# Kernel optimization log

Hardware: AMD Instinct MI355X
Metric: run time of the kernel (lower is better)

## Reference

```python
import jax, jax.numpy as jnp
import numpy as np

D_K = 128


def setup_inputs() -> dict:
    key = jax.random.key(0)
    kq, kk, kv = jax.random.split(key, 3)
    S = 8192
    Query = jax.random.normal(kq, (S, D_K), dtype=jnp.float32)
    Key = jax.random.normal(kk, (S, D_K), dtype=jnp.float32)
    Value = jax.random.normal(kv, (S, D_K), dtype=jnp.float32)
    return {"Query": Query, "Key": Key, "Value": Value}


def reference(Query, Key, Value):
    # scaled dot-product attention, unmasked (masked=False default)
    scale = 1.0 / jnp.sqrt(jnp.asarray(D_K, dtype=jnp.float32))
    scores = jnp.matmul(Query, Key.T) * scale          # [S, S]
    attn = jax.nn.softmax(scores, axis=1)              # softmax over keys (dim=1 on 2-D)
    delta_E = jnp.matmul(attn, Value)                  # [S, d_k]
    return delta_E
```

## Files before the change

### kernel.cpp

```cpp
#include <hip/hip_runtime.h>

#define S_LEN 8192
#define D_KK  128
#define SCALE 0.08838834764831845f

typedef __bf16 bf16x2 __attribute__((ext_vector_type(2)));
typedef __bf16 bf16x4 __attribute__((ext_vector_type(4)));
typedef __bf16 bf16x8 __attribute__((ext_vector_type(8)));
typedef float  f32x16 __attribute__((ext_vector_type(16)));
typedef _Float16 half_t;

__global__ __launch_bounds__(256) void prep_kv_23450521436217(
    const float* __restrict__ K,
    const float* __restrict__ V,
    __bf16* __restrict__ Kf,
    __bf16* __restrict__ Vf)
{
    const int tid = threadIdx.x;
    const int t   = blockIdx.x;
    __shared__ __bf16 T[32][140];

    const float* ktile = K + (size_t)t * 32 * D_KK;
    const float* vtile = V + (size_t)t * 32 * D_KK;

    const int row = tid & 31;
    const int cp  = tid >> 5;
    #pragma unroll
    for (int i = 0; i < 2; ++i) {
        int c = cp * 2 + i;
        int s = c >> 1, hi = c & 1;
        const float* src = ktile + row * D_KK + c * 8;
        float4 a = *(const float4*)(src);
        float4 b = *(const float4*)(src + 4);
        bf16x8 o;
        o[0]=(__bf16)a.x; o[1]=(__bf16)a.y; o[2]=(__bf16)a.z; o[3]=(__bf16)a.w;
        o[4]=(__bf16)b.x; o[5]=(__bf16)b.y; o[6]=(__bf16)b.z; o[7]=(__bf16)b.w;
        *(bf16x8*)(Kf + (size_t)(t * 8 + s) * 512 + hi * 256 + row * 8) = o;
    }

    #pragma unroll
    for (int i = 0; i < 4; ++i) {
        int f4 = tid + i * 256;
        float4 v = ((const float4*)vtile)[f4];
        int r = f4 >> 5, cc = (f4 & 31) << 2;
        bf16x4 b;
        b[0]=(__bf16)v.x; b[1]=(__bf16)v.y; b[2]=(__bf16)v.z; b[3]=(__bf16)v.w;
        *(bf16x4*)(&T[r][cc]) = b;
    }
    __syncthreads();

    #pragma unroll
    for (int i = 0; i < 2; ++i) {
        int idx  = tid + i * 256;
        int frag = idx >> 6, lane = idx & 63;
        int hi = lane >> 5, l5 = lane & 31;
        int d = frag >> 1, h = frag & 1;
        bf16x8 o;
        #pragma unroll
        for (int j = 0; j < 8; ++j) o[j] = T[16 * h + 8 * hi + j][32 * d + l5];
        *(bf16x8*)(Vf + (size_t)(t * 8 + frag) * 512 + lane * 8) = o;
    }
}

__global__ __launch_bounds__(512, 2) void attn_part_23450521436217(
    const float*  __restrict__ Q,
    const __bf16* __restrict__ Kf,
    const __bf16* __restrict__ Vf,
    half_t* __restrict__ P16,
    float*  __restrict__ Mp,
    float*  __restrict__ Lp)
{
    const int tid  = threadIdx.x;
    const int wave = tid >> 6;
    const int lane = tid & 63;
    const int l5   = lane & 31;
    const int hi   = lane >> 5;

    const int ks   = blockIdx.x & 7;
    const int qt   = blockIdx.x >> 3;
    const int qsub = qt * 8 + wave;
    const int qrow = qsub * 32 + l5;

    __shared__ __align__(16) __bf16 Klds[2][4096];

    bf16x8 qf[8];
    #pragma unroll
    for (int s = 0; s < 8; ++s) {
        const float* qp = Q + (size_t)qrow * D_KK + s * 16 + hi * 8;
        float4 a = *(const float4*)(qp);
        float4 b = *(const float4*)(qp + 4);
        bf16x8 f;
        f[0]=(__bf16)(a.x*SCALE); f[1]=(__bf16)(a.y*SCALE);
        f[2]=(__bf16)(a.z*SCALE); f[3]=(__bf16)(a.w*SCALE);
        f[4]=(__bf16)(b.x*SCALE); f[5]=(__bf16)(b.y*SCALE);
        f[6]=(__bf16)(b.z*SCALE); f[7]=(__bf16)(b.w*SCALE);
        qf[s] = f;
    }

    f32x16 oacc[4];
    #pragma unroll
    for (int d = 0; d < 4; ++d) oacc[d] = f32x16{};
    float m_run = -1e30f, l_run = 0.0f;

    const __bf16* kbase = Kf + (size_t)(ks * 32) * 4096;
    const __bf16* vfp   = Vf + (size_t)(ks * 32) * 4096 + lane * 8;

    {
        const __bf16* src = kbase + wave * 512 + lane * 8;
        __builtin_amdgcn_global_load_lds(
            (const __attribute__((address_space(1))) void*)src,
            (__attribute__((address_space(3))) void*)&Klds[0][wave * 512],
            16, 0, 0);
    }
    __syncthreads();

    for (int it = 0; it < 32; ++it) {
        const int cur = it & 1;

        if (it < 31) {
            const __bf16* src = kbase + (size_t)(it + 1) * 4096 + wave * 512 + lane * 8;
            __builtin_amdgcn_global_load_lds(
                (const __attribute__((address_space(1))) void*)src,
                (__attribute__((address_space(3))) void*)&Klds[cur ^ 1][wave * 512],
                16, 0, 0);
        }

        const __bf16* vt = vfp + (size_t)it * 4096;
        bf16x8 vb[8];
        #pragma unroll
        for (int f = 0; f < 8; ++f) vb[f] = *(const bf16x8*)(vt + f * 512);

        f32x16 c = f32x16{};
        __builtin_amdgcn_s_setprio(1);
        #pragma unroll
        for (int s = 0; s < 8; ++s) {
            bf16x8 kf = *(const bf16x8*)(&Klds[cur][s * 512 + lane * 8]);
            c = __builtin_amdgcn_mfma_f32_32x32x16_bf16(kf, qf[s], c, 0, 0, 0);
        }
        __builtin_amdgcn_s_setprio(0);

        float x0 = fmaxf(c[0], c[8]),  x1 = fmaxf(c[1], c[9]);
        float x2 = fmaxf(c[2], c[10]), x3 = fmaxf(c[3], c[11]);
        float x4 = fmaxf(c[4], c[12]), x5 = fmaxf(c[5], c[13]);
        float x6 = fmaxf(c[6], c[14]), x7 = fmaxf(c[7], c[15]);
        float y0 = fmaxf(fmaxf(x0, x4), fmaxf(x1, x5));
        float y1 = fmaxf(fmaxf(x2, x6), fmaxf(x3, x7));
        float tmax = fmaxf(y0, y1);
        tmax = fmaxf(tmax, __shfl_xor(tmax, 32));
        if (__any(tmax > m_run + 8.0f)) {
            float mnew  = fmaxf(m_run, tmax);
            float alpha = __expf(m_run - mnew);
            #pragma unroll
            for (int d = 0; d < 4; ++d) oacc[d] *= alpha;
            l_run *= alpha;
            m_run  = mnew;
        }
        float p[16];
        #pragma unroll
        for (int r = 0; r < 16; ++r) p[r] = __expf(c[r] - m_run);
        float s0a = (p[0]+p[1]) + (p[2]+p[3]),   s1a = (p[4]+p[5]) + (p[6]+p[7]);
        float s2a = (p[8]+p[9]) + (p[10]+p[11]), s3a = (p[12]+p[13]) + (p[14]+p[15]);
        float ps = (s0a + s1a) + (s2a + s3a);
        ps += __shfl_xor(ps, 32);
        l_run += ps;

        unsigned pk[8];
        #pragma unroll
        for (int tq = 0; tq < 8; ++tq) {
            bf16x2 w; w[0] = (__bf16)p[2*tq]; w[1] = (__bf16)p[2*tq+1];
            pk[tq] = __builtin_bit_cast(unsigned, w);
        }
        asm volatile("v_permlane32_swap_b32 %0, %1" : "+v"(pk[0]), "+v"(pk[2]));
        asm volatile("v_permlane32_swap_b32 %0, %1" : "+v"(pk[1]), "+v"(pk[3]));
        asm volatile("v_permlane32_swap_b32 %0, %1" : "+v"(pk[4]), "+v"(pk[6]));
        asm volatile("v_permlane32_swap_b32 %0, %1" : "+v"(pk[5]), "+v"(pk[7]));
        union { unsigned u[4]; bf16x8 f; } b0, b1;
        b0.u[0]=pk[0]; b0.u[1]=pk[1]; b0.u[2]=pk[2]; b0.u[3]=pk[3];
        b1.u[0]=pk[4]; b1.u[1]=pk[5]; b1.u[2]=pk[6]; b1.u[3]=pk[7];

        __builtin_amdgcn_s_setprio(1);
        #pragma unroll
        for (int d = 0; d < 4; ++d) {
            oacc[d] = __builtin_amdgcn_mfma_f32_32x32x16_bf16(vb[2*d+0], b0.f,
                                                              oacc[d], 0,0,0);
            oacc[d] = __builtin_amdgcn_mfma_f32_32x32x16_bf16(vb[2*d+1], b1.f,
                                                              oacc[d], 0,0,0);
        }
        __builtin_amdgcn_s_setprio(0);

        __syncthreads();
    }

    if (lane < 32) {
        Mp[ks * S_LEN + qrow] = m_run;
        Lp[ks * S_LEN + qrow] = l_run;
    }
    half_t* pb = P16 + (size_t)(ks * 256 + qsub) * (128 * 32);
    #pragma unroll
    for (int d = 0; d < 4; ++d)
        #pragma unroll
        for (int reg = 0; reg < 16; ++reg) {
            int drow = d * 32 + (reg & 3) + 8 * (reg >> 2) + 4 * hi;
            pb[drow * 32 + l5] = (half_t)oacc[d][reg];
        }
}

__global__ __launch_bounds__(256) void attn_merge_23450521436217(
    const half_t* __restrict__ P16,
    const float*  __restrict__ Mp,
    const float*  __restrict__ Lp,
    float* __restrict__ O)
{
    const int tid  = threadIdx.x;
    const int qsub = blockIdx.x;

    __shared__ float W[8][32];
    __shared__ float Li[32];
    __shared__ float Ot[128][33];

    if (tid < 32) {
        const int qrow = qsub * 32 + tid;
        float m[8], l[8];
        #pragma unroll
        for (int ks = 0; ks < 8; ++ks) {
            m[ks] = Mp[ks * S_LEN + qrow];
            l[ks] = Lp[ks * S_LEN + qrow];
        }
        float M = m[0];
        #pragma unroll
        for (int ks = 1; ks < 8; ++ks) M = fmaxf(M, m[ks]);
        float L = 0.0f;
        #pragma unroll
        for (int ks = 0; ks < 8; ++ks) {
            float w = __expf(m[ks] - M);
            W[ks][tid] = w;
            L += l[ks] * w;
        }
        Li[tid] = 1.0f / L;
    }
    __syncthreads();

    const int q  = tid & 31;
    const int dg = tid >> 5;
    #pragma unroll
    for (int j = 0; j < 16; ++j) {
        const int d = dg * 16 + j;
        float acc = 0.0f;
        #pragma unroll
        for (int ks = 0; ks < 8; ++ks)
            acc += W[ks][q] *
                   (float)P16[(size_t)(ks * 256 + qsub) * (128 * 32) + d * 32 + q];
        Ot[d][q] = acc;
    }
    __syncthreads();

    const int qq = tid >> 3;
    const int dv = (tid & 7) * 16;
    const float il = Li[qq];
    float* op = O + (size_t)(qsub * 32 + qq) * D_KK + dv;
    #pragma unroll
    for (int i = 0; i < 4; ++i) {
        float4 o;
        o.x = Ot[dv + i*4 + 0][qq] * il;
        o.y = Ot[dv + i*4 + 1][qq] * il;
        o.z = Ot[dv + i*4 + 2][qq] * il;
        o.w = Ot[dv + i*4 + 3][qq] * il;
        ((float4*)op)[i] = o;
    }
}

extern "C" void kernel_launch(void* const* d_in, const int* in_sizes, int n_in,
                              void* d_out, int out_size, void* d_ws, size_t ws_size,
                              hipStream_t stream) {
    const float* Q = (const float*)d_in[0];
    const float* K = (const float*)d_in[1];
    const float* V = (const float*)d_in[2];
    float* O = (float*)d_out;

    char* ws = (char*)d_ws;
    const size_t kf_b = (size_t)S_LEN * D_KK * 2;
    __bf16* Kf = (__bf16*)(ws);
    __bf16* Vf = (__bf16*)(ws + kf_b);
    float*  Mp = (float*) (ws + 2 * kf_b);
    float*  Lp = (float*) (ws + 2 * kf_b + 8 * S_LEN * 4);
    half_t* P16= (half_t*)(ws + 2 * kf_b + 16 * S_LEN * 4);

    hipLaunchKernelGGL(prep_kv_23450521436217, dim3(S_LEN/32), dim3(256), 0, stream,
                       K, V, Kf, Vf);
    hipLaunchKernelGGL(attn_part_23450521436217, dim3(256), dim3(512), 0, stream,
                       Q, Kf, Vf, P16, Mp, Lp);
    hipLaunchKernelGGL(attn_merge_23450521436217, dim3(S_LEN/32), dim3(256), 0, stream,
                       P16, Mp, Lp, O);
}
```

Baseline: 63.83 us.

## Stage V tiles through double-buffered LDS and switch softmax to exp2 domain

V tiles are now streamed into a second double-buffered LDS array with async global-to-LDS loads, alongside K. Previously every wave fetched its own V fragments from global memory straight into registers, so the same data was loaded eight times per block. Separately, log2(e) is folded into the Q scale so the softmax can use exp2f instead of __expf, and the rescale threshold becomes 11.5, which is 8 in natural-log units. The change doubles LDS use per block, which may lower occupancy, and adds LDS reads in the PV stage.

```diff
diff --git a/kernel.cpp b/kernel.cpp
--- a/kernel.cpp
+++ b/kernel.cpp
@@ -2,7 +2,7 @@
 
 #define S_LEN 8192
 #define D_KK  128
-#define SCALE 0.08838834764831845f
+#define SCALE2 (0.08838834764831845f * 1.44269504088896340f)
 
 typedef __bf16 bf16x2 __attribute__((ext_vector_type(2)));
 typedef __bf16 bf16x4 __attribute__((ext_vector_type(4)));
@@ -82,6 +82,7 @@
     const int qrow = qsub * 32 + l5;
 
     __shared__ __align__(16) __bf16 Klds[2][4096];
+    __shared__ __align__(16) __bf16 Vlds[2][4096];
 
     bf16x8 qf[8];
     #pragma unroll
@@ -90,10 +91,10 @@
         float4 a = *(const float4*)(qp);
         float4 b = *(const float4*)(qp + 4);
         bf16x8 f;
-        f[0]=(__bf16)(a.x*SCALE); f[1]=(__bf16)(a.y*SCALE);
-        f[2]=(__bf16)(a.z*SCALE); f[3]=(__bf16)(a.w*SCALE);
-        f[4]=(__bf16)(b.x*SCALE); f[5]=(__bf16)(b.y*SCALE);
-        f[6]=(__bf16)(b.z*SCALE); f[7]=(__bf16)(b.w*SCALE);
+        f[0]=(__bf16)(a.x*SCALE2); f[1]=(__bf16)(a.y*SCALE2);
+        f[2]=(__bf16)(a.z*SCALE2); f[3]=(__bf16)(a.w*SCALE2);
+        f[4]=(__bf16)(b.x*SCALE2); f[5]=(__bf16)(b.y*SCALE2);
+        f[6]=(__bf16)(b.z*SCALE2); f[7]=(__bf16)(b.w*SCALE2);
         qf[s] = f;
     }
 
@@ -103,14 +104,19 @@
     float m_run = -1e30f, l_run = 0.0f;
 
     const __bf16* kbase = Kf + (size_t)(ks * 32) * 4096;
-    const __bf16* vfp   = Vf + (size_t)(ks * 32) * 4096 + lane * 8;
+    const __bf16* vbase = Vf + (size_t)(ks * 32) * 4096;
 
     {
-        const __bf16* src = kbase + wave * 512 + lane * 8;
+        const __bf16* ksrc = kbase + wave * 512 + lane * 8;
         __builtin_amdgcn_global_load_lds(
-            (const __attribute__((address_space(1))) void*)src,
+            (const __attribute__((address_space(1))) void*)ksrc,
             (__attribute__((address_space(3))) void*)&Klds[0][wave * 512],
             16, 0, 0);
+        const __bf16* vsrc = vbase + wave * 512 + lane * 8;
+        __builtin_amdgcn_global_load_lds(
+            (const __attribute__((address_space(1))) void*)vsrc,
+            (__attribute__((address_space(3))) void*)&Vlds[0][wave * 512],
+            16, 0, 0);
     }
     __syncthreads();
 
@@ -118,17 +124,17 @@
         const int cur = it & 1;
 
         if (it < 31) {
-            const __bf16* src = kbase + (size_t)(it + 1) * 4096 + wave * 512 + lane * 8;
+            const __bf16* ksrc = kbase + (size_t)(it + 1) * 4096 + wave * 512 + lane * 8;
             __builtin_amdgcn_global_load_lds(
-                (const __attribute__((address_space(1))) void*)src,
+                (const __attribute__((address_space(1))) void*)ksrc,
                 (__attribute__((address_space(3))) void*)&Klds[cur ^ 1][wave * 512],
                 16, 0, 0);
-        }
-
-        const __bf16* vt = vfp + (size_t)it * 4096;
-        bf16x8 vb[8];
-        #pragma unroll
-        for (int f = 0; f < 8; ++f) vb[f] = *(const bf16x8*)(vt + f * 512);
+            const __bf16* vsrc = vbase + (size_t)(it + 1) * 4096 + wave * 512 + lane * 8;
+            __builtin_amdgcn_global_load_lds(
+                (const __attribute__((address_space(1))) void*)vsrc,
+                (__attribute__((address_space(3))) void*)&Vlds[cur ^ 1][wave * 512],
+                16, 0, 0);
+        }
 
         f32x16 c = f32x16{};
         __builtin_amdgcn_s_setprio(1);
@@ -147,9 +153,9 @@
         float y1 = fmaxf(fmaxf(x2, x6), fmaxf(x3, x7));
         float tmax = fmaxf(y0, y1);
         tmax = fmaxf(tmax, __shfl_xor(tmax, 32));
-        if (__any(tmax > m_run + 8.0f)) {
+        if (__any(tmax > m_run + 11.5f)) {
             float mnew  = fmaxf(m_run, tmax);
-            float alpha = __expf(m_run - mnew);
+            float alpha = exp2f(m_run - mnew);
             #pragma unroll
             for (int d = 0; d < 4; ++d) oacc[d] *= alpha;
             l_run *= alpha;
@@ -157,7 +163,7 @@
         }
         float p[16];
         #pragma unroll
-        for (int r = 0; r < 16; ++r) p[r] = __expf(c[r] - m_run);
+        for (int r = 0; r < 16; ++r) p[r] = exp2f(c[r] - m_run);
         float s0a = (p[0]+p[1]) + (p[2]+p[3]),   s1a = (p[4]+p[5]) + (p[6]+p[7]);
         float s2a = (p[8]+p[9]) + (p[10]+p[11]), s3a = (p[12]+p[13]) + (p[14]+p[15]);
         float ps = (s0a + s1a) + (s2a + s3a);
@@ -181,9 +187,11 @@
         __builtin_amdgcn_s_setprio(1);
         #pragma unroll
         for (int d = 0; d < 4; ++d) {
-            oacc[d] = __builtin_amdgcn_mfma_f32_32x32x16_bf16(vb[2*d+0], b0.f,
+            bf16x8 v0 = *(const bf16x8*)(&Vlds[cur][(2*d)     * 512 + lane * 8]);
+            bf16x8 v1 = *(const bf16x8*)(&Vlds[cur][(2*d + 1) * 512 + lane * 8]);
+            oacc[d] = __builtin_amdgcn_mfma_f32_32x32x16_bf16(v0, b0.f,
                                                               oacc[d], 0,0,0);
-            oacc[d] = __builtin_amdgcn_mfma_f32_32x32x16_bf16(vb[2*d+1], b1.f,
+            oacc[d] = __builtin_amdgcn_mfma_f32_32x32x16_bf16(v1, b1.f,
                                                               oacc[d], 0,0,0);
         }
         __builtin_amdgcn_s_setprio(0);
@@ -232,7 +240,7 @@
         float L = 0.0f;
         #pragma unroll
         for (int ks = 0; ks < 8; ++ks) {
-            float w = __expf(m[ks] - M);
+            float w = exp2f(m[ks] - M);
             W[ks][tid] = w;
             L += l[ks] * w;
         }
```

New measurement: 73.03 us. 1.14x slower.

## Process two K/V subtiles per barrier and switch softmax to exp2 domain

Applied to the files above, without the earlier changes.

The main loop now stages two 32-key K subtiles per LDS buffer and runs 16 iterations instead of 32. This halves the number of __syncthreads barriers and prefetches twice as much K data per step. Q is pre-scaled by log2(e) so the softmax and the merge weights can use exp2f instead of __expf, and the rescale threshold is raised to 11.5 to match the base-2 domain. LDS use doubles and register pressure rises because two sets of V fragments are held per iteration, which may lower occupancy.

```diff
diff --git a/kernel.cpp b/kernel.cpp
--- a/kernel.cpp
+++ b/kernel.cpp
@@ -2,7 +2,7 @@
 
 #define S_LEN 8192
 #define D_KK  128
-#define SCALE 0.08838834764831845f
+#define SCALE2 (0.08838834764831845f * 1.44269504088896340f)
 
 typedef __bf16 bf16x2 __attribute__((ext_vector_type(2)));
 typedef __bf16 bf16x4 __attribute__((ext_vector_type(4)));
@@ -81,7 +81,7 @@
     const int qsub = qt * 8 + wave;
     const int qrow = qsub * 32 + l5;
 
-    __shared__ __align__(16) __bf16 Klds[2][4096];
+    __shared__ __align__(16) __bf16 Klds[2][2][4096];
 
     bf16x8 qf[8];
     #pragma unroll
@@ -90,10 +90,10 @@
         float4 a = *(const float4*)(qp);
         float4 b = *(const float4*)(qp + 4);
         bf16x8 f;
-        f[0]=(__bf16)(a.x*SCALE); f[1]=(__bf16)(a.y*SCALE);
-        f[2]=(__bf16)(a.z*SCALE); f[3]=(__bf16)(a.w*SCALE);
-        f[4]=(__bf16)(b.x*SCALE); f[5]=(__bf16)(b.y*SCALE);
-        f[6]=(__bf16)(b.z*SCALE); f[7]=(__bf16)(b.w*SCALE);
+        f[0]=(__bf16)(a.x*SCALE2); f[1]=(__bf16)(a.y*SCALE2);
+        f[2]=(__bf16)(a.z*SCALE2); f[3]=(__bf16)(a.w*SCALE2);
+        f[4]=(__bf16)(b.x*SCALE2); f[5]=(__bf16)(b.y*SCALE2);
+        f[6]=(__bf16)(b.z*SCALE2); f[7]=(__bf16)(b.w*SCALE2);
         qf[s] = f;
     }
 
@@ -105,91 +105,110 @@
     const __bf16* kbase = Kf + (size_t)(ks * 32) * 4096;
     const __bf16* vfp   = Vf + (size_t)(ks * 32) * 4096 + lane * 8;
 
-    {
-        const __bf16* src = kbase + wave * 512 + lane * 8;
+    #pragma unroll
+    for (int st = 0; st < 2; ++st) {
+        const __bf16* src = kbase + (size_t)st * 4096 + wave * 512 + lane * 8;
         __builtin_amdgcn_global_load_lds(
             (const __attribute__((address_space(1))) void*)src,
-            (__attribute__((address_space(3))) void*)&Klds[0][wave * 512],
+            (__attribute__((address_space(3))) void*)&Klds[0][st][wave * 512],
             16, 0, 0);
     }
     __syncthreads();
 
-    for (int it = 0; it < 32; ++it) {
+#define SUBTILE(CUR, ST, IT, VB)                                               \
+    {                                                                          \
+        f32x16 c = f32x16{};                                                   \
+        __builtin_amdgcn_s_setprio(1);                                         \
+        _Pragma("unroll")                                                      \
+        for (int s = 0; s < 8; ++s) {                                          \
+            bf16x8 kf = *(const bf16x8*)(&Klds[CUR][ST][s * 512 + lane * 8]);  \
+            c = __builtin_amdgcn_mfma_f32_32x32x16_bf16(kf, qf[s], c, 0, 0, 0);\
+        }                                                                      \
+        __builtin_amdgcn_s_setprio(0);                                         \
+        float x0 = fmaxf(c[0], c[8]),  x1 = fmaxf(c[1], c[9]);                 \
+        float x2 = fmaxf(c[2], c[10]), x3 = fmaxf(c[3], c[11]);                \
+        float x4 = fmaxf(c[4], c[12]), x5 = fmaxf(c[5], c[13]);                \
+        float x6 = fmaxf(c[6], c[14]), x7 = fmaxf(c[7], c[15]);                \
+        float y0 = fmaxf(fmaxf(x0, x4), fmaxf(x1, x5));                        \
+        float y1 = fmaxf(fmaxf(x2, x6), fmaxf(x3, x7));                        \
+        float tmax = fmaxf(y0, y1);                                            \
+        tmax = fmaxf(tmax, __shfl_xor(tmax, 32));                              \
+        if (__any(tmax > m_run + 11.5f)) {                                     \
+            float mnew  = fmaxf(m_run, tmax);                                  \
+            float alpha = exp2f(m_run - mnew);                                 \
+            _Pragma("unroll")                                                  \
+            for (int d = 0; d < 4; ++d) oacc[d] *= alpha;                      \
+            l_run *= alpha;                                                    \
+            m_run  = mnew;                                                     \
+        }                                                                      \
+        float p[16];                                                           \
+        _Pragma("unroll")                                                      \
+        for (int r = 0; r < 16; ++r) p[r] = exp2f(c[r] - m_run);               \
+        float s0a = (p[0]+p[1]) + (p[2]+p[3]),   s1a = (p[4]+p[5]) + (p[6]+p[7]);   \
+        float s2a = (p[8]+p[9]) + (p[10]+p[11]), s3a = (p[12]+p[13]) + (p[14]+p[15]); \
+        float ps = (s0a + s1a) + (s2a + s3a);                                  \
+        ps += __shfl_xor(ps, 32);                                              \
+        l_run += ps;                                                           \
+        unsigned pk[8];                                                        \
+        _Pragma("unroll")                                                      \
+        for (int tq = 0; tq < 8; ++tq) {                                       \
+            bf16x2 w; w[0] = (__bf16)p[2*tq]; w[1] = (__bf16)p[2*tq+1];        \
+            pk[tq] = __builtin_bit_cast(unsigned, w);                          \
+        }                                                                      \
+        asm volatile("v_permlane32_swap_b32 %0, %1" : "+v"(pk[0]), "+v"(pk[2]));\
+        asm volatile("v_permlane32_swap_b32 %0, %1" : "+v"(pk[1]), "+v"(pk[3]));\
+        asm volatile("v_permlane32_swap_b32 %0, %1" : "+v"(pk[4]), "+v"(pk[6]));\
+        asm volatile("v_permlane32_swap_b32 %0, %1" : "+v"(pk[5]), "+v"(pk[7]));\
+        union { unsigned u[4]; bf16x8 f; } b0, b1;                             \
+        b0.u[0]=pk[0]; b0.u[1]=pk[1]; b0.u[2]=pk[2]; b0.u[3]=pk[3];            \
+        b1.u[0]=pk[4]; b1.u[1]=pk[5]; b1.u[2]=pk[6]; b1.u[3]=pk[7];            \
+        __builtin_amdgcn_s_setprio(1);                                         \
+        _Pragma("unroll")                                                      \
+        for (int d = 0; d < 4; ++d) {                                          \
+            oacc[d] = __builtin_amdgcn_mfma_f32_32x32x16_bf16(VB[2*d+0], b0.f, \
+                                                              oacc[d], 0,0,0); \
+            oacc[d] = __builtin_amdgcn_mfma_f32_32x32x16_bf16(VB[2*d+1], b1.f, \
+                                                              oacc[d], 0,0,0); \
+        }                                                                      \
+        __builtin_amdgcn_s_setprio(0);                                         \
+    }
+
+    for (int it = 0; it < 16; ++it) {
         const int cur = it & 1;
 
-        if (it < 31) {
-            const __bf16* src = kbase + (size_t)(it + 1) * 4096 + wave * 512 + lane * 8;
-            __builtin_amdgcn_global_load_lds(
-                (const __attribute__((address_space(1))) void*)src,
-                (__attribute__((address_space(3))) void*)&Klds[cur ^ 1][wave * 512],
-                16, 0, 0);
-        }
-
-        const __bf16* vt = vfp + (size_t)it * 4096;
-        bf16x8 vb[8];
-        #pragma unroll
-        for (int f = 0; f < 8; ++f) vb[f] = *(const bf16x8*)(vt + f * 512);
-
-        f32x16 c = f32x16{};
-        __builtin_amdgcn_s_setprio(1);
-        #pragma unroll
-        for (int s = 0; s < 8; ++s) {
-            bf16x8 kf = *(const bf16x8*)(&Klds[cur][s * 512 + lane * 8]);
-            c = __builtin_amdgcn_mfma_f32_32x32x16_bf16(kf, qf[s], c, 0, 0, 0);
-        }
-        __builtin_amdgcn_s_setprio(0);
-
-        float x0 = fmaxf(c[0], c[8]),  x1 = fmaxf(c[1], c[9]);
-        float x2 = fmaxf(c[2], c[10]), x3 = fmaxf(c[3], c[11]);
-        float x4 = fmaxf(c[4], c[12]), x5 = fmaxf(c[5], c[13]);
-        float x6 = fmaxf(c[6], c[14]), x7 = fmaxf(c[7], c[15]);
-        float y0 = fmaxf(fmaxf(x0, x4), fmaxf(x1, x5));
-        float y1 = fmaxf(fmaxf(x2, x6), fmaxf(x3, x7));
-        float tmax = fmaxf(y0, y1);
-        tmax = fmaxf(tmax, __shfl_xor(tmax, 32));
-        if (__any(tmax > m_run + 8.0f)) {
-            float mnew  = fmaxf(m_run, tmax);
-            float alpha = __expf(m_run - mnew);
+        if (it < 15) {
             #pragma unroll
-            for (int d = 0; d < 4; ++d) oacc[d] *= alpha;
-            l_run *= alpha;
-            m_run  = mnew;
-        }
-        float p[16];
-        #pragma unroll
-        for (int r = 0; r < 16; ++r) p[r] = __expf(c[r] - m_run);
-        float s0a = (p[0]+p[1]) + (p[2]+p[3]),   s1a = (p[4]+p[5]) + (p[6]+p[7]);
-        float s2a = (p[8]+p[9]) + (p[10]+p[11]), s3a = (p[12]+p[13]) + (p[14]+p[15]);
-        float ps = (s0a + s1a) + (s2a + s3a);
-        ps += __shfl_xor(ps, 32);
-        l_run += ps;
-
-        unsigned pk[8];
-        #pragma unroll
-        for (int tq = 0; tq < 8; ++tq) {
-            bf16x2 w; w[0] = (__bf16)p[2*tq]; w[1] = (__bf16)p[2*tq+1];
-            pk[tq] = __builtin_bit_cast(unsigned, w);
-        }
-        asm volatile("v_permlane32_swap_b32 %0, %1" : "+v"(pk[0]), "+v"(pk[2]));
-        asm volatile("v_permlane32_swap_b32 %0, %1" : "+v"(pk[1]), "+v"(pk[3]));
-        asm volatile("v_permlane32_swap_b32 %0, %1" : "+v"(pk[4]), "+v"(pk[6]));
-        asm volatile("v_permlane32_swap_b32 %0, %1" : "+v"(pk[5]), "+v"(pk[7]));
-        union { unsigned u[4]; bf16x8 f; } b0, b1;
-        b0.u[0]=pk[0]; b0.u[1]=pk[1]; b0.u[2]=pk[2]; b0.u[3]=pk[3];
-        b1.u[0]=pk[4]; b1.u[1]=pk[5]; b1.u[2]=pk[6]; b1.u[3]=pk[7];
-
-        __builtin_amdgcn_s_setprio(1);
-        #pragma unroll
-        for (int d = 0; d < 4; ++d) {
-            oacc[d] = __builtin_amdgcn_mfma_f32_32x32x16_bf16(vb[2*d+0], b0.f,
-                                                              oacc[d], 0,0,0);
-            oacc[d] = __builtin_amdgcn_mfma_f32_32x32x16_bf16(vb[2*d+1], b1.f,
-                                                              oacc[d], 0,0,0);
-        }
-        __builtin_amdgcn_s_setprio(0);
+            for (int st = 0; st < 2; ++st) {
+                const __bf16* src = kbase + (size_t)(2*it + 2 + st) * 4096
+                                  + wave * 512 + lane * 8;
+                __builtin_amdgcn_global_load_lds(
+                    (const __attribute__((address_space(1))) void*)src,
+                    (__attribute__((address_space(3))) void*)&Klds[cur ^ 1][st][wave * 512],
+                    16, 0, 0);
+            }
+        }
+
+        bf16x8 vbA[8];
+        {
+            const __bf16* vt = vfp + (size_t)(2*it) * 4096;
+            #pragma unroll
+            for (int f = 0; f < 8; ++f) vbA[f] = *(const bf16x8*)(vt + f * 512);
+        }
+
+        SUBTILE(cur, 0, it, vbA)
+
+        bf16x8 vbB[8];
+        {
+            const __bf16* vt = vfp + (size_t)(2*it + 1) * 4096;
+            #pragma unroll
+            for (int f = 0; f < 8; ++f) vbB[f] = *(const bf16x8*)(vt + f * 512);
+        }
+
+        SUBTILE(cur, 1, it, vbB)
 
         __syncthreads();
     }
+#undef SUBTILE
 
     if (lane < 32) {
         Mp[ks * S_LEN + qrow] = m_run;
@@ -232,7 +251,7 @@
         float L = 0.0f;
         #pragma unroll
         for (int ks = 0; ks < 8; ++ks) {
-            float w = __expf(m[ks] - M);
+            float w = exp2f(m[ks] - M);
             W[ks][tid] = w;
             L += l[ks] * w;
         }
```

After: 66.96 us. 4.9% more time.
